# Kernel tuning notes

Measured on AMD Instinct MI355X. Metric: run time of the kernel, lower is better.

The kernel has to match this reference:

```python
import jax, jax.numpy as jnp
import numpy as np

# MX fp8 (e4m3) element-format parameters
BLOCK = 32
EBITS = 4
MBITS = 5                      # sign+implicit+3 explicit mantissa bits (microxcaling convention)
EMAX = 8                       # e4m3 special case: emax = 2**(ebits-1)
MAX_NORM = 448.0               # e4m3 max finite magnitude (saturating cast)
MIN_EXP = -(2 ** (EBITS - 1)) + 2   # -6, smallest normal exponent
SCALE_EMAX = 127.0             # e8m0 shared-exponent range
TINY = np.float32(np.finfo(np.float32).tiny)


def mx_fp8_fake_quant(x):
    """Block-wise shared-exponent (MX) fp8-e4m3 fake quantization.

    Returns (qdq, shared_exp) where qdq has the shape/dtype of x and
    shared_exp is the per-block e8m0 exponent (float, pre-bias).
    """
    shape = x.shape
    xb = x.reshape(-1, BLOCK)                                  # [n_blocks, 32]
    amax = jnp.max(jnp.abs(xb), axis=-1, keepdims=True)        # per-block amax
    shared_exp = jnp.floor(jnp.log2(jnp.where(amax == 0, TINY, amax))) - EMAX
    shared_exp = jnp.clip(shared_exp, -SCALE_EMAX, SCALE_EMAX)
    scale = jnp.exp2(shared_exp)
    xs = xb / scale                                            # scaled into element range
    # element-wise quantize to the e4m3 grid
    absx = jnp.abs(xs)
    priv_exp = jnp.maximum(jnp.floor(jnp.log2(jnp.where(absx == 0, TINY, absx))), MIN_EXP)
    pscale = jnp.exp2(priv_exp - (MBITS - 2))                  # quantum = 2^(e-3)
    q = jnp.round(xs / pscale) * pscale                        # round-half-even mantissa
    q = jnp.clip(q, -MAX_NORM, MAX_NORM)                       # saturate
    return (q * scale).reshape(shape), shared_exp


def setup_inputs() -> dict:
    key = jax.random.key(0)
    inputs = jax.random.normal(key, (8192, 8192), dtype=jnp.float32)
    return {"inputs": inputs}


def reference(inputs):
    # TensorQuantizer.forward: fake-quantize, cast back to input dtype.
    q, _shared_exp = mx_fp8_fake_quant(inputs)
    return q.astype(inputs.dtype)
```

## Files before the change

kernel.cpp:

```cpp
#include <hip/hip_runtime.h>


__global__ __launch_bounds__(256) void mx_fp8_qdq_kernel(
    const float4* __restrict__ in, float4* __restrict__ out, int n4) {
  int i = blockIdx.x * blockDim.x + threadIdx.x;
  if (i >= n4) return;

  float4 v = in[i];

  float a = fmaxf(fmaxf(fabsf(v.x), fabsf(v.y)), fmaxf(fabsf(v.z), fabsf(v.w)));
  a = fmaxf(a, __shfl_xor(a, 1, 8));
  a = fmaxf(a, __shfl_xor(a, 2, 8));
  a = fmaxf(a, __shfl_xor(a, 4, 8));

  int eb = (int)((__float_as_uint(a) >> 23) & 0xFF);
  if (eb < 1) eb = 1;
  int s = eb - 127 - 8;
  if (s < -127) s = -127;

  const float inv_scale = __uint_as_float((unsigned)(127 - s) << 23);

  #define QDQ1(x)                                                              \
    ({                                                                         \
      float xs_ = (x) * inv_scale;                                             \
      int pe_ = (int)((__float_as_uint(xs_) >> 23) & 0xFF);                    \
      pe_ = (pe_ < 1 ? 1 : pe_) - 127;                                         \
      if (pe_ < -6) pe_ = -6;                                                  \
                              \
      float ips_ = __uint_as_float((unsigned)(130 - pe_) << 23);               \
      float r_ = rintf(xs_ * ips_);              \
      float ps_ = __uint_as_float((unsigned)(124 + pe_) << 23);  \
      float q_ = r_ * ps_;                        \
      q_ = fminf(fmaxf(q_, -448.0f), 448.0f);                                  \
      ldexpf(q_, s);                                 \
    })

  float4 o;
  o.x = QDQ1(v.x);
  o.y = QDQ1(v.y);
  o.z = QDQ1(v.z);
  o.w = QDQ1(v.w);
  #undef QDQ1

  out[i] = o;
}

extern "C" void kernel_launch(void* const* d_in, const int* in_sizes, int n_in,
                              void* d_out, int out_size, void* d_ws, size_t ws_size,
                              hipStream_t stream) {
  const float4* in = (const float4*)d_in[0];
  float4* out = (float4*)d_out;
  int n4 = in_sizes[0] / 4;
  int block = 256;
  int grid = (n4 + block - 1) / block;
  mx_fp8_qdq_kernel<<<grid, block, 0, stream>>>(in, out, n4);
}
```

Before: 410.7 us.

## Batch four float4 loads per thread and use DPP for block amax

Each thread now issues four strided float4 loads up front before processing them, so more memory requests are in flight per wave while the grid shrinks by the same factor. The 8-lane amax reduction switches from __shfl_xor (ds_bpermute through LDS hardware) to DPP lane-permute intrinsics, which avoid the LDS path. This adds register pressure and relies on the DPP patterns covering exactly the 8-lane groups.

```diff
diff --git a/kernel.cpp b/kernel.cpp
--- a/kernel.cpp
+++ b/kernel.cpp
@@ -1,48 +1,71 @@
 #include <hip/hip_runtime.h>
 
 
+#define UNROLL 4
+
+__device__ __forceinline__ float dpp_max8(float a) {
+  int t;
+  t = __builtin_amdgcn_update_dpp(0, __float_as_int(a), 0xB1, 0xF, 0xF, true);
+  a = fmaxf(a, __int_as_float(t));
+  t = __builtin_amdgcn_update_dpp(0, __float_as_int(a), 0x4E, 0xF, 0xF, true);
+  a = fmaxf(a, __int_as_float(t));
+  t = __builtin_amdgcn_update_dpp(0, __float_as_int(a), 0x141, 0xF, 0xF, true);
+  a = fmaxf(a, __int_as_float(t));
+  return a;
+}
+
+__device__ __forceinline__ float qdq1(float x, float inv_scale, int s) {
+  float xs = x * inv_scale;
+  int pe = (int)((__float_as_uint(xs) >> 23) & 0xFF);
+  pe = (pe < 1 ? 1 : pe) - 127;
+  if (pe < -6) pe = -6;
+  float ips = __uint_as_float((unsigned)(130 - pe) << 23);
+  float r = rintf(xs * ips);
+  float ps = __uint_as_float((unsigned)(124 + pe) << 23);
+  float q = r * ps;
+  q = fminf(fmaxf(q, -448.0f), 448.0f);
+  return ldexpf(q, s);
+}
+
 __global__ __launch_bounds__(256) void mx_fp8_qdq_kernel(
     const float4* __restrict__ in, float4* __restrict__ out, int n4) {
-  int i = blockIdx.x * blockDim.x + threadIdx.x;
-  if (i >= n4) return;
+  const int stride = gridDim.x * blockDim.x;
+  const int i0 = blockIdx.x * blockDim.x + threadIdx.x;
 
-  float4 v = in[i];
+  int idx[UNROLL];
+  float4 v[UNROLL];
+  bool ok[UNROLL];
 
-  float a = fmaxf(fmaxf(fabsf(v.x), fabsf(v.y)), fmaxf(fabsf(v.z), fabsf(v.w)));
-  a = fmaxf(a, __shfl_xor(a, 1, 8));
-  a = fmaxf(a, __shfl_xor(a, 2, 8));
-  a = fmaxf(a, __shfl_xor(a, 4, 8));
+#pragma unroll
+  for (int j = 0; j < UNROLL; ++j) {
+    idx[j] = i0 + j * stride;
+    ok[j] = idx[j] < n4;
+    if (ok[j]) v[j] = in[idx[j]];
+  }
 
-  int eb = (int)((__float_as_uint(a) >> 23) & 0xFF);
-  if (eb < 1) eb = 1;
-  int s = eb - 127 - 8;
-  if (s < -127) s = -127;
+#pragma unroll
+  for (int j = 0; j < UNROLL; ++j) {
+    if (!ok[j]) continue;
+    float4 x = v[j];
 
-  const float inv_scale = __uint_as_float((unsigned)(127 - s) << 23);
+    float a = fmaxf(fmaxf(fabsf(x.x), fabsf(x.y)),
+                    fmaxf(fabsf(x.z), fabsf(x.w)));
+    a = dpp_max8(a);
 
-  #define QDQ1(x)                                                              \
-    ({                                                                         \
-      float xs_ = (x) * inv_scale;                                             \
-      int pe_ = (int)((__float_as_uint(xs_) >> 23) & 0xFF);                    \
-      pe_ = (pe_ < 1 ? 1 : pe_) - 127;                                         \
-      if (pe_ < -6) pe_ = -6;                                                  \
-                              \
-      float ips_ = __uint_as_float((unsigned)(130 - pe_) << 23);               \
-      float r_ = rintf(xs_ * ips_);              \
-      float ps_ = __uint_as_float((unsigned)(124 + pe_) << 23);  \
-      float q_ = r_ * ps_;                        \
-      q_ = fminf(fmaxf(q_, -448.0f), 448.0f);                                  \
-      ldexpf(q_, s);                                 \
-    })
+    int eb = (int)((__float_as_uint(a) >> 23) & 0xFF);
+    if (eb < 1) eb = 1;
+    int s = eb - 135;
+    if (s < -127) s = -127;
 
-  float4 o;
-  o.x = QDQ1(v.x);
-  o.y = QDQ1(v.y);
-  o.z = QDQ1(v.z);
-  o.w = QDQ1(v.w);
-  #undef QDQ1
+    const float inv_scale = __uint_as_float((unsigned)(127 - s) << 23);
 
-  out[i] = o;
+    float4 o;
+    o.x = qdq1(x.x, inv_scale, s);
+    o.y = qdq1(x.y, inv_scale, s);
+    o.z = qdq1(x.z, inv_scale, s);
+    o.w = qdq1(x.w, inv_scale, s);
+    out[idx[j]] = o;
+  }
 }
 
 extern "C" void kernel_launch(void* const* d_in, const int* in_sizes, int n_in,
@@ -52,6 +75,7 @@
   float4* out = (float4*)d_out;
   int n4 = in_sizes[0] / 4;
   int block = 256;
-  int grid = (n4 + block - 1) / block;
+  int per_block = block * UNROLL;
+  int grid = (n4 + per_block - 1) / per_block;
   mx_fp8_qdq_kernel<<<grid, block, 0, stream>>>(in, out, n4);
 }
```

After: 428.6 us. +4.4%, slower.
